# Optimization experiments

Hardware: AMD Instinct MI355X
Metric: run time of the kernel (lower is better)

The kernel has to match this reference:

```python
import jax, jax.numpy as jnp
import numpy as np

B, S, HIDDEN, HEADS = 2, 1024, 1024, 8
HEAD = HIDDEN // HEADS
EPS = 1e-5


def setup_inputs() -> dict:
    key = jax.random.key(0)
    ks = jax.random.split(key, 11)
    d = HEAD
    return {
        "X": jax.random.normal(ks[0], (B, S, HIDDEN), jnp.float32),
        "Wq": jax.random.normal(ks[1], (HEADS, d, d), jnp.float32) / d,
        "Wk": jax.random.normal(ks[2], (HEADS, d, d), jnp.float32) / d,
        "Wv": jax.random.normal(ks[3], (HEADS, d, d), jnp.float32) / d,
        "theta": jax.random.normal(ks[4], (HEADS, d), jnp.float32) / d,
        "gn_weight": jnp.ones((HIDDEN,), jnp.float32),
        "gn_bias": jnp.zeros((HIDDEN,), jnp.float32),
        "Wg_re": jax.random.normal(ks[5], (HIDDEN, HIDDEN), jnp.float32) / HIDDEN,
        "Wg_im": jax.random.normal(ks[6], (HIDDEN, HIDDEN), jnp.float32) / HIDDEN,
        "Wo_re": jax.random.normal(ks[7], (HIDDEN, HIDDEN), jnp.float32) / HIDDEN,
        "Wo_im": jax.random.normal(ks[8], (HIDDEN, HIDDEN), jnp.float32) / HIDDEN,
    }


def _head(Xh, Wq, Wk, Wv, theta, gamma):
    # Xh: [B, S, d] complex64; one retention head with decay gamma.
    c = Xh.dtype
    s = Xh.shape[1]
    ns = jnp.arange(1, s + 1, dtype=jnp.float32)
    phase = ns[:, None] * theta[None, :]            # [S, d]
    Theta = jnp.exp(1j * phase).astype(c)           # exp(i*n*theta)
    Q = (Xh @ Wq.astype(c)) * Theta[None]
    K = (Xh @ Wk.astype(c)) * jnp.conj(Theta)[None]
    V = Xh @ Wv.astype(c)
    diff = ns[:, None] - ns[None, :]                # n - m
    D = jnp.where(diff >= 0, gamma ** jnp.maximum(diff, 0.0), 0.0).astype(c)
    att = jnp.einsum('bnd,bmd->bnm', Q, K) * D[None]  # no conjugation (plain matmul, as in torch)
    return jnp.einsum('bnm,bmd->bnd', att, V)


def _group_norm(Y, w, b):
    # complex group norm: per-group complex mean, real variance E|x-mu|^2 (unbiased)
    Z = Y.reshape(-1, HEADS, HEAD)
    mu = Z.mean(axis=2, keepdims=True)
    dz = Z - mu
    var = (dz.real ** 2 + dz.imag ** 2).sum(axis=2, keepdims=True) / (HEAD - 1)
    Z = dz / jnp.sqrt(var + EPS).astype(Z.dtype)
    Z = Z.reshape(-1, HIDDEN)
    return Z * w + b


def _forward(X, Wq, Wk, Wv, theta, gn_weight, gn_bias, Wg_re, Wg_im, Wo_re, Wo_im):
    c = jnp.complex64
    Xc = X.astype(c)
    gammas = (1.0 - jnp.exp(jnp.linspace(np.log(1.0 / 32.0), np.log(1.0 / 512.0), HEADS))).astype(jnp.float32)
    Xh = Xc.reshape(B, S, HEADS, HEAD).transpose(2, 0, 1, 3)  # [H, B, S, d]
    Y = jax.vmap(_head)(Xh, Wq, Wk, Wv, theta, gammas)        # [H, B, S, d]
    Y = Y.transpose(1, 2, 0, 3).reshape(B, S, HIDDEN)         # concat heads
    Y = _group_norm(Y.reshape(-1, HIDDEN), gn_weight, gn_bias).reshape(B, S, HIDDEN)
    Wg = (Wg_re + 1j * Wg_im).astype(c)
    Wo = (Wo_re + 1j * Wo_im).astype(c)
    G = Xc @ Wg
    G = G * (1.0 / (1.0 + jnp.exp(-G)))                       # complex swish
    return (G + Y) @ Wo


def reference(X, Wq, Wk, Wv, theta, gn_weight, gn_bias, Wg_re, Wg_im, Wo_re, Wo_im):
    return _forward(X, Wq, Wk, Wv, theta, gn_weight, gn_bias, Wg_re, Wg_im, Wo_re, Wo_im)
```

## Files before the change

kernel.cpp:

```cpp
#include <hip/hip_runtime.h>
#include <math.h>

#define BATCH  2
#define SEQ    1024
#define HIDDEN 1024
#define NHEADS 8
#define DHEAD  128
#define NTOK   (BATCH*SEQ)
#define GEPS   1e-5f

typedef float f32x16 __attribute__((ext_vector_type(16)));
typedef __bf16 bf16x8 __attribute__((ext_vector_type(8)));
typedef unsigned int u32x4 __attribute__((ext_vector_type(4)));
typedef unsigned int u32x2 __attribute__((ext_vector_type(2)));

union Frag { u32x4 u; bf16x8 h; };

__device__ __forceinline__ unsigned short f2bf(float f) {
    unsigned int u = __float_as_uint(f);
    unsigned int r = (u + 0x7FFFu + ((u >> 16) & 1u)) >> 16;
    return (unsigned short)r;
}
__device__ __forceinline__ float bf2f(unsigned short u) {
    return __uint_as_float(((unsigned int)u) << 16);
}

__device__ __forceinline__ void cswish(float zr, float zi, float& outr, float& outi) {
    const float e = expf(-zr);
    float sg, cg;
    sincosf(zi, &sg, &cg);
    const float wr = fmaf(e, cg, 1.0f);
    const float wi = -e*sg;
    const float inv = 1.0f / fmaf(wr, wr, wi*wi);
    outr = (zr*wr + zi*wi)*inv;
    outi = (zi*wr - zr*wi)*inv;
}

__global__ __launch_bounds__(256) void prep_kernel(
    const float* __restrict__ X,
    const float* __restrict__ Wq, const float* __restrict__ Wk, const float* __restrict__ Wv,
    const float* __restrict__ Wgre, const float* __restrict__ Wgim,
    const float* __restrict__ Wore, const float* __restrict__ Woim,
    float* __restrict__ gpow, unsigned short* __restrict__ Xb,
    unsigned short* __restrict__ Wt, unsigned short* __restrict__ Bg,
    unsigned short* __restrict__ Bot)
{
    __shared__ float Ws[64][65];
    const int id  = blockIdx.x;
    const int tid = threadIdx.x;

    if (id < 32) {
        const int h = id >> 2;
        const int k = (id & 3)*256 + tid;
        const float l = fmaf((float)h, -0.39608410317711170f, -3.46573590279972650f);
        const float gamma = 1.0f - expf(l);
        gpow[h*SEQ + k] = powf(gamma, (float)k);
    } else if (id < 1056) {
        const size_t i = ((size_t)(id - 32)*256 + tid)*8;
        const float4 a = *(const float4*)&X[i];
        const float4 b = *(const float4*)&X[i+4];
        __align__(16) unsigned short t[8] = { f2bf(a.x), f2bf(a.y), f2bf(a.z), f2bf(a.w),
                                              f2bf(b.x), f2bf(b.y), f2bf(b.z), f2bf(b.w) };
        *(u32x4*)&Xb[i] = *(u32x4*)t;
    } else if (id < 1152) {
        const int q = id - 1056;
        const int th_ = q % 24, yy = q / 24;
        const int type = th_ >> 3, h = th_ & 7;
        const int k0 = (yy >> 1)*64, n0 = (yy & 1)*64;
        const float* W = ((type == 0) ? Wq : (type == 1) ? Wk : Wv)
                         + (size_t)h*DHEAD*DHEAD;
        #pragma unroll
        for (int it = 0; it < 4; ++it) {
            const int r = (tid >> 4) + it*16, c = (tid & 15)*4;
            *(float4*)&Ws[r][c] = *(const float4*)&W[(size_t)(k0 + r)*DHEAD + n0 + c];
        }
        __syncthreads();
        const int nl = tid >> 2, seg = (tid & 3)*16;
        __align__(16) unsigned short t[16];
        #pragma unroll
        for (int j = 0; j < 16; ++j) t[j] = f2bf(Ws[seg + j][nl]);
        u32x4* d = (u32x4*)&Wt[((size_t)th_*DHEAD + n0 + nl)*DHEAD + k0 + seg];
        d[0] = ((u32x4*)t)[0];
        d[1] = ((u32x4*)t)[1];
    } else if (id < 1664) {
        const int q = id - 1152;
        const int xx = q & 31, k0 = (q >> 5)*64;
        const int plane = xx >> 4;
        const int c0 = (xx & 15)*64;
        const float* src = plane ? Wgim : Wgre;
        #pragma unroll
        for (int it = 0; it < 4; ++it) {
            const int r = (tid >> 4) + it*16, c = (tid & 15)*4;
            *(float4*)&Ws[r][c] = *(const float4*)&src[(size_t)(k0 + r)*HIDDEN + c0 + c];
        }
        __syncthreads();
        const int nl = tid >> 2, seg = (tid & 3)*16;
        __align__(16) unsigned short t[16];
        #pragma unroll
        for (int j = 0; j < 16; ++j) t[j] = f2bf(Ws[seg + j][nl]);
        u32x4* d = (u32x4*)&Bg[((size_t)plane << 20) + (size_t)(c0 + nl)*HIDDEN + k0 + seg];
        d[0] = ((u32x4*)t)[0];
        d[1] = ((u32x4*)t)[1];
    } else {
        const int q = id - 1664;
        const int n0 = (q & 15)*64, k0 = (q >> 4)*64;
        const float* src;
        float sign = 1.0f;
        if (k0 < HIDDEN) src = Wore; else { src = Woim; sign = -1.0f; }
        const int kc = k0 & (HIDDEN-1);
        #pragma unroll
        for (int it = 0; it < 4; ++it) {
            const int r = (tid >> 4) + it*16, c = (tid & 15)*4;
            const float4 v = *(const float4*)&src[(size_t)(kc + r)*HIDDEN + n0 + c];
            Ws[r][c+0] = v.x*sign; Ws[r][c+1] = v.y*sign; Ws[r][c+2] = v.z*sign; Ws[r][c+3] = v.w*sign;
        }
        __syncthreads();
        const int nl = tid >> 2, seg = (tid & 3)*16;
        __align__(16) unsigned short t[16];
        #pragma unroll
        for (int j = 0; j < 16; ++j) t[j] = f2bf(Ws[seg + j][nl]);
        u32x4* d = (u32x4*)&Bot[(size_t)(n0 + nl)*(2*HIDDEN) + k0 + seg];
        d[0] = ((u32x4*)t)[0];
        d[1] = ((u32x4*)t)[1];
    }
}

__global__ __launch_bounds__(256) void projm_kernel(
    const unsigned short* __restrict__ Xb,
    const unsigned short* __restrict__ Wt,
    const float* __restrict__ theta,
    unsigned short* __restrict__ Qbre, unsigned short* __restrict__ Qbim,
    unsigned short* __restrict__ Kbre, unsigned short* __restrict__ Kbim,
    unsigned short* __restrict__ Vtb)
{
    const int tt = blockIdx.x;
    const int h  = blockIdx.y;
    const int mt = blockIdx.z;
    const int tid = threadIdx.x;
    const int w = tid >> 6, lane = tid & 63;
    const int th = w >> 1, nh = w & 1;
    const int l31 = lane & 31, hi = (lane >> 5) & 1;

    Frag A[8];
    {
        const unsigned short* xa = Xb + (size_t)(tt*64 + th*32 + l31)*HIDDEN
                                   + h*DHEAD + 8*hi;
        #pragma unroll
        for (int ks = 0; ks < 8; ++ks) A[ks].u = *(const u32x4*)(xa + 16*ks);
    }

    const unsigned short* wb = Wt + (size_t)(mt*NHEADS + h)*DHEAD*DHEAD;

    #pragma unroll
    for (int nt = 0; nt < 2; ++nt) {
        const int n0 = nh*64 + nt*32;
        const int n  = n0 + l31;

        Frag B[8];
        const unsigned short* wp = wb + (size_t)n*DHEAD + 8*hi;
        #pragma unroll
        for (int ks = 0; ks < 8; ++ks) B[ks].u = *(const u32x4*)(wp + 16*ks);

        f32x16 acc;
        #pragma unroll
        for (int e = 0; e < 16; ++e) acc[e] = 0.f;
        #pragma unroll
        for (int ks = 0; ks < 8; ++ks)
            acc = __builtin_amdgcn_mfma_f32_32x32x16_bf16(A[ks].h, B[ks].h, acc, 0, 0, 0);

        if (mt == 2) {
            const int b2  = (tt*64) >> 10;
            const int bh2 = b2*NHEADS + h;
            const int sbase = (tt*64 + th*32) & (SEQ-1);
            unsigned short* vdst = Vtb + ((size_t)(bh2*DHEAD + n))*SEQ + sbase;
            #pragma unroll
            for (int g2 = 0; g2 < 4; ++g2) {
                const int s0 = 8*g2 + 4*hi;
                __align__(8) unsigned short t4[4];
                #pragma unroll
                for (int j = 0; j < 4; ++j) t4[j] = f2bf(acc[g2*4 + j]);
                *(u32x2*)(vdst + s0) = *(u32x2*)t4;
            }
        } else {
            const float thv = theta[h*DHEAD + n];
            unsigned short* pre = (mt == 0) ? Qbre : Kbre;
            unsigned short* pim = (mt == 0) ? Qbim : Kbim;
            const float sgn = (mt == 0) ? 1.0f : -1.0f;
            #pragma unroll
            for (int r = 0; r < 16; ++r) {
                const int row = (r & 3) + 8*(r >> 2) + 4*hi;
                const int tok = tt*64 + th*32 + row;
                const float np1 = (float)((tok & (SEQ-1)) + 1);
                float s, c;
                sincosf(np1*thv, &s, &c);
                const size_t g = (size_t)tok*HIDDEN + h*DHEAD + n;
                pre[g] = f2bf(acc[r]*c);
                pim[g] = f2bf(acc[r]*s*sgn);
            }
        }
    }
}

#define CVTPK(dst, a, b) asm("v_cvt_pk_bf16_f32 %0, %1, %2" : "=v"(dst) : "v"(a), "v"(b))
#define SWAP32(x, y)     asm("v_permlane32_swap_b32 %0, %1" : "+v"(x), "+v"(y))

union FatLds {
    struct { float Ytr[32][133]; float Yti[32][133]; } a;
    struct { unsigned short As[64][68]; unsigned short Br[64][68]; unsigned short Bi[64][68]; } g;
};

__global__ __launch_bounds__(128) void fat_kernel(
    const unsigned short* __restrict__ Qbre, const unsigned short* __restrict__ Qbim,
    const unsigned short* __restrict__ Kbre, const unsigned short* __restrict__ Kbim,
    const unsigned short* __restrict__ Vtb,  const float* __restrict__ gpow,
    const float* __restrict__ gnw, const float* __restrict__ gnb,
    unsigned short* __restrict__ Yn,
    const unsigned short* __restrict__ Xb, const unsigned short* __restrict__ Bg,
    unsigned short* __restrict__ Gs)
{
    __shared__ FatLds lds;

    const int bid  = blockIdx.x;
    const int tid  = threadIdx.x;
    const int lane = tid & 63;
    const int wv   = tid >> 6;
    const int l31 = lane & 31, hi = (lane >> 5) & 1;

    if (bid < 512) {
        const int id = bid;
        const int bh = ((id & 7) << 1) | ((id >> 3) & 1);
        const int qt = id >> 4;

        const int b = bh >> 3, h = bh & 7;
        const int q0 = qt * 32;
        const size_t bhoff = (size_t)b*SEQ*HIDDEN + h*DHEAD;
        const float* gp = gpow + h*SEQ;

        int   crw[16];
        float ginv[16];
        #pragma unroll
        for (int r = 0; r < 16; ++r) {
            const int cr = (r & 3) + 8*(r >> 2) + 4*hi;
            crw[r] = cr;
            ginv[r] = 1.0f / gp[cr];
        }

        Frag Qr[8], Qi[8];
        {
            const unsigned short* qr = Qbre + bhoff + (size_t)(q0 + l31)*HIDDEN + 8*hi;
            const unsigned short* qi = Qbim + bhoff + (size_t)(q0 + l31)*HIDDEN + 8*hi;
            #pragma unroll
            for (int ks = 0; ks < 8; ++ks) {
                Qr[ks].u = *(const u32x4*)(qr + 16*ks);
                Qi[ks].u = *(const u32x4*)(qi + 16*ks);
            }
        }

        f32x16 Yr[4], Yi[4];
        #pragma unroll
        for (int dt = 0; dt < 4; ++dt)
            #pragma unroll
            for (int e = 0; e < 16; ++e) { Yr[dt][e] = 0.f; Yi[dt][e] = 0.f; }

        const int nm   = qt + 1;
        const int half = (nm + 1) >> 1;
        const int mlo  = wv ? half : 0;
        const int mhi  = wv ? nm   : half;

        #pragma unroll 1
        for (int m = mlo; m < mhi; ++m) {
            const int kv0 = m*32;

            Frag Kr[8], Ki[8];
            {
                const unsigned short* kr = Kbre + bhoff + (size_t)(kv0 + l31)*HIDDEN + 8*hi;
                const unsigned short* ki = Kbim + bhoff + (size_t)(kv0 + l31)*HIDDEN + 8*hi;
                #pragma unroll
                for (int ks = 0; ks < 8; ++ks) {
                    Kr[ks].u = *(const u32x4*)(kr + 16*ks);
                    Ki[ks].u = *(const u32x4*)(ki + 16*ks);
                }
            }
            Frag Vf[4][2];
            #pragma unroll
            for (int dt = 0; dt < 4; ++dt)
                #pragma unroll
                for (int ks2 = 0; ks2 < 2; ++ks2)
                    Vf[dt][ks2].u = *(const u32x4*)(Vtb + ((size_t)(bh*DHEAD + dt*32 + l31))*SEQ
                                                    + kv0 + 16*ks2 + 8*hi);

            const int  base = 32*(qt - m) + l31;
            const float g1  = gp[base];

            f32x16 SR, SI;
            #pragma unroll
            for (int e = 0; e < 16; ++e) { SR[e] = 0.f; SI[e] = 0.f; }
            #pragma unroll
            for (int ks = 0; ks < 8; ++ks) {
                Frag Qin;
                #pragma unroll
                for (int e = 0; e < 4; ++e) Qin.u[e] = Qi[ks].u[e] ^ 0x80008000u;
                SR = __builtin_amdgcn_mfma_f32_32x32x16_bf16(Kr[ks].h, Qr[ks].h, SR, 0, 0, 0);
                SI = __builtin_amdgcn_mfma_f32_32x32x16_bf16(Kr[ks].h, Qi[ks].h, SI, 0, 0, 0);
                SR = __builtin_amdgcn_mfma_f32_32x32x16_bf16(Ki[ks].h, Qin.h, SR, 0, 0, 0);
                SI = __builtin_amdgcn_mfma_f32_32x32x16_bf16(Ki[ks].h, Qr[ks].h, SI, 0, 0, 0);
            }

            float pr[16], pi[16];
            #pragma unroll
            for (int r = 0; r < 16; ++r) {
                const float w = (base >= crw[r]) ? g1*ginv[r] : 0.0f;
                pr[r] = SR[r]*w;
                pi[r] = SI[r]*w;
            }

            Frag PR[2], PI[2];
            #pragma unroll
            for (int ks2 = 0; ks2 < 2; ++ks2) {
                const int o = ks2*8;
                unsigned int a0, b0, a1, b1;
                CVTPK(a0, pr[o+0], pr[o+1]);
                CVTPK(b0, pr[o+4], pr[o+5]);
                SWAP32(a0, b0);
                CVTPK(a1, pr[o+2], pr[o+3]);
                CVTPK(b1, pr[o+6], pr[o+7]);
                SWAP32(a1, b1);
                PR[ks2].u[0] = a0; PR[ks2].u[1] = a1; PR[ks2].u[2] = b0; PR[ks2].u[3] = b1;
                CVTPK(a0, pi[o+0], pi[o+1]);
                CVTPK(b0, pi[o+4], pi[o+5]);
                SWAP32(a0, b0);
                CVTPK(a1, pi[o+2], pi[o+3]);
                CVTPK(b1, pi[o+6], pi[o+7]);
                SWAP32(a1, b1);
                PI[ks2].u[0] = a0; PI[ks2].u[1] = a1; PI[ks2].u[2] = b0; PI[ks2].u[3] = b1;
            }

            #pragma unroll
            for (int dt = 0; dt < 4; ++dt) {
                Yr[dt] = __builtin_amdgcn_mfma_f32_32x32x16_bf16(Vf[dt][0].h, PR[0].h, Yr[dt], 0, 0, 0);
                Yr[dt] = __builtin_amdgcn_mfma_f32_32x32x16_bf16(Vf[dt][1].h, PR[1].h, Yr[dt], 0, 0, 0);
                Yi[dt] = __builtin_amdgcn_mfma_f32_32x32x16_bf16(Vf[dt][0].h, PI[0].h, Yi[dt], 0, 0, 0);
                Yi[dt] = __builtin_amdgcn_mfma_f32_32x32x16_bf16(Vf[dt][1].h, PI[1].h, Yi[dt], 0, 0, 0);
            }
        }

        if (wv == 0) {
            #pragma unroll
            for (int dt = 0; dt < 4; ++dt)
                #pragma unroll
                for (int r = 0; r < 16; ++r) {
                    lds.a.Ytr[l31][dt*32 + crw[r]] = Yr[dt][r];
                    lds.a.Yti[l31][dt*32 + crw[r]] = Yi[dt][r];
                }
        }
        __syncthreads();
        if (wv == 1) {
            #pragma unroll
            for (int dt = 0; dt < 4; ++dt)
                #pragma unroll
                for (int r = 0; r < 16; ++r) {
                    lds.a.Ytr[l31][dt*32 + crw[r]] += Yr[dt][r];
                    lds.a.Yti[l31][dt*32 + crw[r]] += Yi[dt][r];
                }
        }
        __syncthreads();

        {
            const int row = tid >> 2;
            const int q4  = tid & 3;
            float sr = 0.f, si = 0.f;
            #pragma unroll 8
            for (int i = 0; i < 32; ++i) {
                sr += lds.a.Ytr[row][q4*32 + i];
                si += lds.a.Yti[row][q4*32 + i];
            }
            sr += __shfl_xor(sr, 1); sr += __shfl_xor(sr, 2);
            si += __shfl_xor(si, 1); si += __shfl_xor(si, 2);
            const float mr = sr * (1.0f/128.0f), mi = si * (1.0f/128.0f);
            float vs = 0.f;
            #pragma unroll 8
            for (int i = 0; i < 32; ++i) {
                const float dr = lds.a.Ytr[row][q4*32 + i] - mr;
                const float di = lds.a.Yti[row][q4*32 + i] - mi;
                vs = fmaf(dr, dr, vs);
                vs = fmaf(di, di, vs);
            }
            vs += __shfl_xor(vs, 1); vs += __shfl_xor(vs, 2);
            const float scale = 1.0f / sqrtf(vs * (1.0f/127.0f) + GEPS);

            unsigned short* dst = Yn + (size_t)(b*SEQ + q0 + row)*(2*HIDDEN) + h*DHEAD + q4*32;
            #pragma unroll
            for (int i = 0; i < 32; i += 8) {
                __align__(16) unsigned short tre[8], tim[8];
                #pragma unroll
                for (int e = 0; e < 8; ++e) {
                    const int col = q4*32 + i + e;
                    const float wv_ = gnw[h*DHEAD + col];
                    const float bv_ = gnb[h*DHEAD + col];
                    tre[e] = f2bf(fmaf((lds.a.Ytr[row][col] - mr)*scale, wv_, bv_));
                    tim[e] = f2bf((lds.a.Yti[row][col] - mi)*scale*wv_);
                }
                *(u32x4*)(dst + i)          = *(u32x4*)tre;
                *(u32x4*)(dst + HIDDEN + i) = *(u32x4*)tim;
            }
        }
    } else {
        const int gid = bid - 512;
        const int mb = gid >> 4;
        const int cb = gid & 15;
        const int wm = wv*32;

        const int arow = tid >> 1, aseg = (tid & 1)*32;
        const unsigned short* ga  = Xb + (size_t)(mb*64 + arow)*HIDDEN + aseg;
        const unsigned short* gbr = Bg + (size_t)(cb*64 + arow)*HIDDEN + aseg;
        const unsigned short* gbi = gbr + (1u << 20);

        f32x16 aR0, aR1, aI0, aI1;
        #pragma unroll
        for (int e = 0; e < 16; ++e) { aR0[e]=0.f; aR1[e]=0.f; aI0[e]=0.f; aI1[e]=0.f; }

        u32x4 ra0 = *(const u32x4*)(ga);
        u32x4 ra1 = *(const u32x4*)(ga + 8);
        u32x4 ra2 = *(const u32x4*)(ga + 16);
        u32x4 ra3 = *(const u32x4*)(ga + 24);
        u32x4 rr0 = *(const u32x4*)(gbr);
        u32x4 rr1 = *(const u32x4*)(gbr + 8);
        u32x4 rr2 = *(const u32x4*)(gbr + 16);
        u32x4 rr3 = *(const u32x4*)(gbr + 24);
        u32x4 ri0 = *(const u32x4*)(gbi);
        u32x4 ri1 = *(const u32x4*)(gbi + 8);
        u32x4 ri2 = *(const u32x4*)(gbi + 16);
        u32x4 ri3 = *(const u32x4*)(gbi + 24);

        for (int kk = 0; kk < HIDDEN; kk += 64) {
            __syncthreads();
            *(u32x4*)&lds.g.As[arow][aseg]      = ra0;
            *(u32x4*)&lds.g.As[arow][aseg + 8]  = ra1;
            *(u32x4*)&lds.g.As[arow][aseg + 16] = ra2;
            *(u32x4*)&lds.g.As[arow][aseg + 24] = ra3;
            *(u32x4*)&lds.g.Br[arow][aseg]      = rr0;
            *(u32x4*)&lds.g.Br[arow][aseg + 8]  = rr1;
            *(u32x4*)&lds.g.Br[arow][aseg + 16] = rr2;
            *(u32x4*)&lds.g.Br[arow][aseg + 24] = rr3;
            *(u32x4*)&lds.g.Bi[arow][aseg]      = ri0;
            *(u32x4*)&lds.g.Bi[arow][aseg + 8]  = ri1;
            *(u32x4*)&lds.g.Bi[arow][aseg + 16] = ri2;
            *(u32x4*)&lds.g.Bi[arow][aseg + 24] = ri3;
            if (kk + 64 < HIDDEN) {
                const int o = kk + 64;
                ra0 = *(const u32x4*)(ga + o);
                ra1 = *(const u32x4*)(ga + o + 8);
                ra2 = *(const u32x4*)(ga + o + 16);
                ra3 = *(const u32x4*)(ga + o + 24);
                rr0 = *(const u32x4*)(gbr + o);
                rr1 = *(const u32x4*)(gbr + o + 8);
                rr2 = *(const u32x4*)(gbr + o + 16);
                rr3 = *(const u32x4*)(gbr + o + 24);
                ri0 = *(const u32x4*)(gbi + o);
                ri1 = *(const u32x4*)(gbi + o + 8);
                ri2 = *(const u32x4*)(gbi + o + 16);
                ri3 = *(const u32x4*)(gbi + o + 24);
            }
            __syncthreads();
            #pragma unroll
            for (int ks = 0; ks < 4; ++ks) {
                Frag a, br0, br1, bi0, bi1;
                a.u   = *(const u32x4*)&lds.g.As[wm + l31][ks*16 + hi*8];
                br0.u = *(const u32x4*)&lds.g.Br[l31     ][ks*16 + hi*8];
                br1.u = *(const u32x4*)&lds.g.Br[l31 + 32][ks*16 + hi*8];
                bi0.u = *(const u32x4*)&lds.g.Bi[l31     ][ks*16 + hi*8];
                bi1.u = *(const u32x4*)&lds.g.Bi[l31 + 32][ks*16 + hi*8];
                aR0 = __builtin_amdgcn_mfma_f32_32x32x16_bf16(a.h, br0.h, aR0, 0, 0, 0);
                aR1 = __builtin_amdgcn_mfma_f32_32x32x16_bf16(a.h, br1.h, aR1, 0, 0, 0);
                aI0 = __builtin_amdgcn_mfma_f32_32x32x16_bf16(a.h, bi0.h, aI0, 0, 0, 0);
                aI1 = __builtin_amdgcn_mfma_f32_32x32x16_bf16(a.h, bi1.h, aI1, 0, 0, 0);
            }
        }

        #pragma unroll
        for (int ct = 0; ct < 2; ++ct) {
            const f32x16& cr = ct ? aR1 : aR0;
            const f32x16& ci = ct ? aI1 : aI0;
            const int c = cb*64 + ct*32 + l31;
            #pragma unroll
            for (int r = 0; r < 16; ++r) {
                const int row = mb*64 + wm + (r & 3) + 8*(r >> 2) + 4*hi;
                float swr, swi;
                cswish(cr[r], ci[r], swr, swi);
                const size_t o = (size_t)row*(2*HIDDEN) + c;
                Gs[o]          = f2bf(swr);
                Gs[o + HIDDEN] = f2bf(swi);
            }
        }
    }
}

__global__ __launch_bounds__(256) void zadd_kernel(
    const unsigned short* __restrict__ Gs, const unsigned short* __restrict__ Yn,
    unsigned short* __restrict__ Aout)
{
    const size_t i = ((size_t)blockIdx.x*256 + threadIdx.x)*8;
    const u32x4 g = *(const u32x4*)&Gs[i];
    const u32x4 y = *(const u32x4*)&Yn[i];
    __align__(16) unsigned short gg[8], yy[8], t[8];
    *(u32x4*)gg = g; *(u32x4*)yy = y;
    #pragma unroll
    for (int e = 0; e < 8; ++e) t[e] = f2bf(bf2f(gg[e]) + bf2f(yy[e]));
    *(u32x4*)&Aout[i] = *(u32x4*)t;
}

__global__ __launch_bounds__(256) void wprep_o_kernel(
    const float* __restrict__ Wore, const float* __restrict__ Woim,
    unsigned short* __restrict__ Bot, const int imMode)
{
    const int n0 = blockIdx.x*64, k0 = blockIdx.y*64;
    const float* src;
    float sign = 1.0f;
    if (!imMode) { if (k0 < HIDDEN) src = Wore; else { src = Woim; sign = -1.0f; } }
    else         { src = (k0 < HIDDEN) ? Woim : Wore; }
    const int kc = k0 & (HIDDEN-1);
    __shared__ float Ws[64][65];
    const int tid = threadIdx.x;
    #pragma unroll
    for (int it = 0; it < 4; ++it) {
        const int r = (tid >> 4) + it*16, c = (tid & 15)*4;
        const float4 v = *(const float4*)&src[(size_t)(kc + r)*HIDDEN + n0 + c];
        Ws[r][c+0] = v.x*sign; Ws[r][c+1] = v.y*sign; Ws[r][c+2] = v.z*sign; Ws[r][c+3] = v.w*sign;
    }
    __syncthreads();
    const int nl = tid >> 2, seg = (tid & 3)*16;
    __align__(16) unsigned short t[16];
    #pragma unroll
    for (int j = 0; j < 16; ++j) t[j] = f2bf(Ws[seg + j][nl]);
    u32x4* d = (u32x4*)&Bot[(size_t)(n0 + nl)*(2*HIDDEN) + k0 + seg];
    d[0] = ((u32x4*)t)[0];
    d[1] = ((u32x4*)t)[1];
}

__global__ __launch_bounds__(256) void ogemm_kernel(
    const unsigned short* __restrict__ A,
    const unsigned short* __restrict__ Bt,
    float* __restrict__ C, const int mode)
{
    const int K = 2*HIDDEN, N = HIDDEN;
    __shared__ __align__(16) unsigned short As[128][72];
    __shared__ __align__(16) unsigned short Bs[64][72];

    const int tid = threadIdx.x;
    const int mb = blockIdx.x, nb = blockIdx.y;
    const int lane = tid & 63, w = tid >> 6;
    const int l31 = lane & 31, hi = (lane >> 5) & 1;
    const int wm = w*32;

    const int arow = tid >> 1, aseg = (tid & 1)*32;
    const int brow = tid >> 2, bseg = (tid & 3)*16;

    const unsigned short* ga = A  + (size_t)(mb*128 + arow)*K + aseg;
    const unsigned short* gb = Bt + (size_t)(nb*64 + brow)*K + bseg;

    f32x16 acc0, acc1;
    #pragma unroll
    for (int e = 0; e < 16; ++e) { acc0[e]=0.f; acc1[e]=0.f; }

    u32x4 ra0 = *(const u32x4*)(ga);
    u32x4 ra1 = *(const u32x4*)(ga + 8);
    u32x4 ra2 = *(const u32x4*)(ga + 16);
    u32x4 ra3 = *(const u32x4*)(ga + 24);
    u32x4 rb0 = *(const u32x4*)(gb);
    u32x4 rb1 = *(const u32x4*)(gb + 8);

    for (int kk = 0; kk < K; kk += 64) {
        __syncthreads();
        *(u32x4*)&As[arow][aseg]      = ra0;
        *(u32x4*)&As[arow][aseg + 8]  = ra1;
        *(u32x4*)&As[arow][aseg + 16] = ra2;
        *(u32x4*)&As[arow][aseg + 24] = ra3;
        *(u32x4*)&Bs[brow][bseg]      = rb0;
        *(u32x4*)&Bs[brow][bseg + 8]  = rb1;
        if (kk + 64 < K) {
            const int o = kk + 64;
            ra0 = *(const u32x4*)(ga + o);
            ra1 = *(const u32x4*)(ga + o + 8);
            ra2 = *(const u32x4*)(ga + o + 16);
            ra3 = *(const u32x4*)(ga + o + 24);
            rb0 = *(const u32x4*)(gb + o);
            rb1 = *(const u32x4*)(gb + o + 8);
        }
        __syncthreads();
        #pragma unroll
        for (int ks = 0; ks < 4; ++ks) {
            Frag a, b0, b1;
            a.u  = *(const u32x4*)&As[wm + l31][ks*16 + hi*8];
            b0.u = *(const u32x4*)&Bs[l31     ][ks*16 + hi*8];
            b1.u = *(const u32x4*)&Bs[l31 + 32][ks*16 + hi*8];
            acc0 = __builtin_amdgcn_mfma_f32_32x32x16_bf16(a.h, b0.h, acc0, 0, 0, 0);
            acc1 = __builtin_amdgcn_mfma_f32_32x32x16_bf16(a.h, b1.h, acc1, 0, 0, 0);
        }
    }

    const int cb = nb*64 + l31;
    #pragma unroll
    for (int r = 0; r < 16; ++r) {
        const int row = mb*128 + wm + (r & 3) + 8*(r >> 2) + 4*hi;
        if (mode == 0) {
            float* cr = C + (size_t)row*N + cb;
            cr[0]  = acc0[r];
            cr[32] = acc1[r];
        } else {
            float* cr = C + ((size_t)row*N + cb)*2 + (mode - 1);
            cr[0]  = acc0[r];
            cr[64] = acc1[r];
        }
    }
}

extern "C" void kernel_launch(void* const* d_in, const int* in_sizes, int n_in,
                              void* d_out, int out_size, void* d_ws, size_t ws_size,
                              hipStream_t stream)
{
    (void)in_sizes; (void)n_in; (void)ws_size;

    const float* X     = (const float*)d_in[0];
    const float* Wq    = (const float*)d_in[1];
    const float* Wk    = (const float*)d_in[2];
    const float* Wv    = (const float*)d_in[3];
    const float* theta = (const float*)d_in[4];
    const float* gnw   = (const float*)d_in[5];
    const float* gnb   = (const float*)d_in[6];
    const float* Wgre  = (const float*)d_in[7];
    const float* Wgim  = (const float*)d_in[8];
    const float* Wore  = (const float*)d_in[9];
    const float* Woim  = (const float*)d_in[10];

    float* ws = (float*)d_ws;
    const size_t P = (size_t)NTOK*HIDDEN;

    unsigned short* Yn   = (unsigned short*)ws;
    unsigned short* Bot  = (unsigned short*)(ws + P);
    unsigned short* Qbre = (unsigned short*)(ws + 2*P);
    unsigned short* Qbim = Qbre + P;
    unsigned short* Kbre = Qbim + P;
    unsigned short* Kbim = Kbre + P;
    unsigned short* Aout = Qbre;
    unsigned short* Gs   = (unsigned short*)(ws + 4*P);
    unsigned short* Vtb  = (unsigned short*)(ws + 5*P);
    unsigned short* Xb   = (unsigned short*)(ws + 5*P) + P;
    unsigned short* Bg   = (unsigned short*)(ws + 6*P);
    unsigned short* Wt   = (unsigned short*)(ws + 6*P) + P;
    unsigned short* Boti = Wt;
    float* gpw = ws + 7*P;

    const int cplx = (out_size >= (int)(2*P)) ? 1 : 0;

    hipLaunchKernelGGL(prep_kernel, dim3(2176), dim3(256), 0, stream,
                       X, Wq, Wk, Wv, Wgre, Wgim, Wore, Woim,
                       gpw, Xb, Wt, Bg, Bot);
    hipLaunchKernelGGL(projm_kernel, dim3(NTOK/64, NHEADS, 3), dim3(256), 0, stream,
                       Xb, Wt, theta, Qbre, Qbim, Kbre, Kbim, Vtb);

    hipLaunchKernelGGL(fat_kernel, dim3(1024), dim3(128), 0, stream,
                       Qbre, Qbim, Kbre, Kbim, Vtb, gpw, gnw, gnb, Yn, Xb, Bg, Gs);

    hipLaunchKernelGGL(zadd_kernel, dim3(2048), dim3(256), 0, stream, Gs, Yn, Aout);

    if (!cplx) {
        hipLaunchKernelGGL(ogemm_kernel, dim3(NTOK/128, HIDDEN/64), dim3(256), 0, stream,
                           Aout, Bot, (float*)d_out, 0);
    } else {
        hipLaunchKernelGGL(wprep_o_kernel, dim3(HIDDEN/64, 2*HIDDEN/64), dim3(256), 0, stream,
                           Wore, Woim, Boti, 1);
        hipLaunchKernelGGL(ogemm_kernel, dim3(NTOK/128, HIDDEN/64), dim3(256), 0, stream,
                           Aout, Bot, (float*)d_out, 1);
        hipLaunchKernelGGL(ogemm_kernel, dim3(NTOK/128, HIDDEN/64), dim3(256), 0, stream,
                           Aout, Boti, (float*)d_out, 2);
    }
}
```

Before: 122.4 us.

## Restructure fat kernel to 4-wave blocks with paired causal tiles and K prefetch

The retention part now uses 256-thread blocks. Each block handles a complementary pair of query tiles (j and 31-j) to balance causal work, and splits the KV range across four waves. K fragments for the next KV tile are loaded early so the loads overlap the MFMAs. The gate GEMM part is re-split into 2x2 waves per 64x64 tile with a swizzled column-block order, and the grid drops from 1024 to 768 blocks. In exchange, the four-wave LDS reduction adds more syncthreads, and larger blocks may lower occupancy.

```diff
diff --git a/kernel.cpp b/kernel.cpp
--- a/kernel.cpp
+++ b/kernel.cpp
@@ -209,7 +209,7 @@
     struct { unsigned short As[64][68]; unsigned short Br[64][68]; unsigned short Bi[64][68]; } g;
 };
 
-__global__ __launch_bounds__(128) void fat_kernel(
+__global__ __launch_bounds__(256) void fat_kernel(
     const unsigned short* __restrict__ Qbre, const unsigned short* __restrict__ Qbim,
     const unsigned short* __restrict__ Kbre, const unsigned short* __restrict__ Kbim,
     const unsigned short* __restrict__ Vtb,  const float* __restrict__ gpow,
@@ -226,13 +226,10 @@
     const int wv   = tid >> 6;
     const int l31 = lane & 31, hi = (lane >> 5) & 1;
 
-    if (bid < 512) {
-        const int id = bid;
-        const int bh = ((id & 7) << 1) | ((id >> 3) & 1);
-        const int qt = id >> 4;
-
+    if (bid < 256) {
+        const int bh = ((bid & 7) << 1) | ((bid >> 3) & 1);
+        const int j  = bid >> 4;
         const int b = bh >> 3, h = bh & 7;
-        const int q0 = qt * 32;
         const size_t bhoff = (size_t)b*SEQ*HIDDEN + h*DHEAD;
         const float* gp = gpow + h*SEQ;
 
@@ -245,248 +242,264 @@
             ginv[r] = 1.0f / gp[cr];
         }
 
-        Frag Qr[8], Qi[8];
-        {
-            const unsigned short* qr = Qbre + bhoff + (size_t)(q0 + l31)*HIDDEN + 8*hi;
-            const unsigned short* qi = Qbim + bhoff + (size_t)(q0 + l31)*HIDDEN + 8*hi;
-            #pragma unroll
-            for (int ks = 0; ks < 8; ++ks) {
-                Qr[ks].u = *(const u32x4*)(qr + 16*ks);
-                Qi[ks].u = *(const u32x4*)(qi + 16*ks);
-            }
-        }
-
-        f32x16 Yr[4], Yi[4];
-        #pragma unroll
-        for (int dt = 0; dt < 4; ++dt)
-            #pragma unroll
-            for (int e = 0; e < 16; ++e) { Yr[dt][e] = 0.f; Yi[dt][e] = 0.f; }
-
-        const int nm   = qt + 1;
-        const int half = (nm + 1) >> 1;
-        const int mlo  = wv ? half : 0;
-        const int mhi  = wv ? nm   : half;
-
         #pragma unroll 1
-        for (int m = mlo; m < mhi; ++m) {
-            const int kv0 = m*32;
-
-            Frag Kr[8], Ki[8];
+        for (int tile = 0; tile < 2; ++tile) {
+            const int qt = tile ? (31 - j) : j;
+            const int q0 = qt * 32;
+
+            Frag Qr[8], Qi[8];
             {
-                const unsigned short* kr = Kbre + bhoff + (size_t)(kv0 + l31)*HIDDEN + 8*hi;
-                const unsigned short* ki = Kbim + bhoff + (size_t)(kv0 + l31)*HIDDEN + 8*hi;
+                const unsigned short* qr = Qbre + bhoff + (size_t)(q0 + l31)*HIDDEN + 8*hi;
+                const unsigned short* qi = Qbim + bhoff + (size_t)(q0 + l31)*HIDDEN + 8*hi;
                 #pragma unroll
                 for (int ks = 0; ks < 8; ++ks) {
-                    Kr[ks].u = *(const u32x4*)(kr + 16*ks);
-                    Ki[ks].u = *(const u32x4*)(ki + 16*ks);
-                }
-            }
-            Frag Vf[4][2];
+                    Qr[ks].u = *(const u32x4*)(qr + 16*ks);
+                    Qi[ks].u = *(const u32x4*)(qi + 16*ks);
+                }
+            }
+
+            f32x16 Yr[4], Yi[4];
             #pragma unroll
             for (int dt = 0; dt < 4; ++dt)
                 #pragma unroll
-                for (int ks2 = 0; ks2 < 2; ++ks2)
-                    Vf[dt][ks2].u = *(const u32x4*)(Vtb + ((size_t)(bh*DHEAD + dt*32 + l31))*SEQ
-                                                    + kv0 + 16*ks2 + 8*hi);
-
-            const int  base = 32*(qt - m) + l31;
-            const float g1  = gp[base];
-
-            f32x16 SR, SI;
-            #pragma unroll
-            for (int e = 0; e < 16; ++e) { SR[e] = 0.f; SI[e] = 0.f; }
-            #pragma unroll
-            for (int ks = 0; ks < 8; ++ks) {
-                Frag Qin;
-                #pragma unroll
-                for (int e = 0; e < 4; ++e) Qin.u[e] = Qi[ks].u[e] ^ 0x80008000u;
-                SR = __builtin_amdgcn_mfma_f32_32x32x16_bf16(Kr[ks].h, Qr[ks].h, SR, 0, 0, 0);
-                SI = __builtin_amdgcn_mfma_f32_32x32x16_bf16(Kr[ks].h, Qi[ks].h, SI, 0, 0, 0);
-                SR = __builtin_amdgcn_mfma_f32_32x32x16_bf16(Ki[ks].h, Qin.h, SR, 0, 0, 0);
-                SI = __builtin_amdgcn_mfma_f32_32x32x16_bf16(Ki[ks].h, Qr[ks].h, SI, 0, 0, 0);
-            }
-
-            float pr[16], pi[16];
-            #pragma unroll
-            for (int r = 0; r < 16; ++r) {
-                const float w = (base >= crw[r]) ? g1*ginv[r] : 0.0f;
-                pr[r] = SR[r]*w;
-                pi[r] = SI[r]*w;
-            }
-
-            Frag PR[2], PI[2];
-            #pragma unroll
-            for (int ks2 = 0; ks2 < 2; ++ks2) {
-                const int o = ks2*8;
-                unsigned int a0, b0, a1, b1;
-                CVTPK(a0, pr[o+0], pr[o+1]);
-                CVTPK(b0, pr[o+4], pr[o+5]);
-                SWAP32(a0, b0);
-                CVTPK(a1, pr[o+2], pr[o+3]);
-                CVTPK(b1, pr[o+6], pr[o+7]);
-                SWAP32(a1, b1);
-                PR[ks2].u[0] = a0; PR[ks2].u[1] = a1; PR[ks2].u[2] = b0; PR[ks2].u[3] = b1;
-                CVTPK(a0, pi[o+0], pi[o+1]);
-                CVTPK(b0, pi[o+4], pi[o+5]);
-                SWAP32(a0, b0);
-                CVTPK(a1, pi[o+2], pi[o+3]);
-                CVTPK(b1, pi[o+6], pi[o+7]);
-                SWAP32(a1, b1);
-                PI[ks2].u[0] = a0; PI[ks2].u[1] = a1; PI[ks2].u[2] = b0; PI[ks2].u[3] = b1;
-            }
-
-            #pragma unroll
-            for (int dt = 0; dt < 4; ++dt) {
-                Yr[dt] = __builtin_amdgcn_mfma_f32_32x32x16_bf16(Vf[dt][0].h, PR[0].h, Yr[dt], 0, 0, 0);
-                Yr[dt] = __builtin_amdgcn_mfma_f32_32x32x16_bf16(Vf[dt][1].h, PR[1].h, Yr[dt], 0, 0, 0);
-                Yi[dt] = __builtin_amdgcn_mfma_f32_32x32x16_bf16(Vf[dt][0].h, PI[0].h, Yi[dt], 0, 0, 0);
-                Yi[dt] = __builtin_amdgcn_mfma_f32_32x32x16_bf16(Vf[dt][1].h, PI[1].h, Yi[dt], 0, 0, 0);
-            }
-        }
-
-        if (wv == 0) {
-            #pragma unroll
-            for (int dt = 0; dt < 4; ++dt)
+                for (int e = 0; e < 16; ++e) { Yr[dt][e] = 0.f; Yi[dt][e] = 0.f; }
+
+            const int nm  = qt + 1;
+            const int mlo = (nm * wv) >> 2;
+            const int mhi = (nm * (wv + 1)) >> 2;
+
+            Frag Kr[8], Ki[8];
+            if (mlo < mhi) {
+                const int kv0p = mlo*32;
+                const unsigned short* kr_ = Kbre + bhoff + (size_t)(kv0p + l31)*HIDDEN + 8*hi;
+                const unsigned short* ki_ = Kbim + bhoff + (size_t)(kv0p + l31)*HIDDEN + 8*hi;
+                #pragma unroll
+                for (int ks = 0; ks < 8; ++ks) {
+                    Kr[ks].u = *(const u32x4*)(kr_ + 16*ks);
+                    Ki[ks].u = *(const u32x4*)(ki_ + 16*ks);
+                }
+            }
+
+            #pragma unroll 1
+            for (int m = mlo; m < mhi; ++m) {
+                const int kv0 = m*32;
+
+                Frag Vf[4][2];
+                #pragma unroll
+                for (int dt = 0; dt < 4; ++dt)
+                    #pragma unroll
+                    for (int ks2 = 0; ks2 < 2; ++ks2)
+                        Vf[dt][ks2].u = *(const u32x4*)(Vtb + ((size_t)(bh*DHEAD + dt*32 + l31))*SEQ
+                                                        + kv0 + 16*ks2 + 8*hi);
+
+                const int  base = 32*(qt - m) + l31;
+                const float g1  = gp[base];
+
+                f32x16 SR, SI;
+                #pragma unroll
+                for (int e = 0; e < 16; ++e) { SR[e] = 0.f; SI[e] = 0.f; }
+                #pragma unroll
+                for (int ks = 0; ks < 8; ++ks) {
+                    Frag Qin;
+                    #pragma unroll
+                    for (int e = 0; e < 4; ++e) Qin.u[e] = Qi[ks].u[e] ^ 0x80008000u;
+                    SR = __builtin_amdgcn_mfma_f32_32x32x16_bf16(Kr[ks].h, Qr[ks].h, SR, 0, 0, 0);
+                    SI = __builtin_amdgcn_mfma_f32_32x32x16_bf16(Kr[ks].h, Qi[ks].h, SI, 0, 0, 0);
+                    SR = __builtin_amdgcn_mfma_f32_32x32x16_bf16(Ki[ks].h, Qin.h, SR, 0, 0, 0);
+                    SI = __builtin_amdgcn_mfma_f32_32x32x16_bf16(Ki[ks].h, Qr[ks].h, SI, 0, 0, 0);
+                }
+
+                if (m + 1 < mhi) {
+                    const int kn = (m + 1)*32;
+                    const unsigned short* kr_ = Kbre + bhoff + (size_t)(kn + l31)*HIDDEN + 8*hi;
+                    const unsigned short* ki_ = Kbim + bhoff + (size_t)(kn + l31)*HIDDEN + 8*hi;
+                    #pragma unroll
+                    for (int ks = 0; ks < 8; ++ks) {
+                        Kr[ks].u = *(const u32x4*)(kr_ + 16*ks);
+                        Ki[ks].u = *(const u32x4*)(ki_ + 16*ks);
+                    }
+                }
+
+                float pr[16], pi[16];
                 #pragma unroll
                 for (int r = 0; r < 16; ++r) {
-                    lds.a.Ytr[l31][dt*32 + crw[r]] = Yr[dt][r];
-                    lds.a.Yti[l31][dt*32 + crw[r]] = Yi[dt][r];
-                }
-        }
-        __syncthreads();
-        if (wv == 1) {
-            #pragma unroll
-            for (int dt = 0; dt < 4; ++dt)
-                #pragma unroll
-                for (int r = 0; r < 16; ++r) {
-                    lds.a.Ytr[l31][dt*32 + crw[r]] += Yr[dt][r];
-                    lds.a.Yti[l31][dt*32 + crw[r]] += Yi[dt][r];
-                }
-        }
-        __syncthreads();
-
-        {
-            const int row = tid >> 2;
-            const int q4  = tid & 3;
-            float sr = 0.f, si = 0.f;
-            #pragma unroll 8
-            for (int i = 0; i < 32; ++i) {
-                sr += lds.a.Ytr[row][q4*32 + i];
-                si += lds.a.Yti[row][q4*32 + i];
-            }
-            sr += __shfl_xor(sr, 1); sr += __shfl_xor(sr, 2);
-            si += __shfl_xor(si, 1); si += __shfl_xor(si, 2);
-            const float mr = sr * (1.0f/128.0f), mi = si * (1.0f/128.0f);
-            float vs = 0.f;
-            #pragma unroll 8
-            for (int i = 0; i < 32; ++i) {
-                const float dr = lds.a.Ytr[row][q4*32 + i] - mr;
-                const float di = lds.a.Yti[row][q4*32 + i] - mi;
-                vs = fmaf(dr, dr, vs);
-                vs = fmaf(di, di, vs);
-            }
-            vs += __shfl_xor(vs, 1); vs += __shfl_xor(vs, 2);
-            const float scale = 1.0f / sqrtf(vs * (1.0f/127.0f) + GEPS);
-
-            unsigned short* dst = Yn + (size_t)(b*SEQ + q0 + row)*(2*HIDDEN) + h*DHEAD + q4*32;
-            #pragma unroll
-            for (int i = 0; i < 32; i += 8) {
-                __align__(16) unsigned short tre[8], tim[8];
-                #pragma unroll
-                for (int e = 0; e < 8; ++e) {
-                    const int col = q4*32 + i + e;
-                    const float wv_ = gnw[h*DHEAD + col];
-                    const float bv_ = gnb[h*DHEAD + col];
-                    tre[e] = f2bf(fmaf((lds.a.Ytr[row][col] - mr)*scale, wv_, bv_));
-                    tim[e] = f2bf((lds.a.Yti[row][col] - mi)*scale*wv_);
-                }
-                *(u32x4*)(dst + i)          = *(u32x4*)tre;
-                *(u32x4*)(dst + HIDDEN + i) = *(u32x4*)tim;
+                    const float w = (base >= crw[r]) ? g1*ginv[r] : 0.0f;
+                    pr[r] = SR[r]*w;
+                    pi[r] = SI[r]*w;
+                }
+
+                Frag PR[2], PI[2];
+                #pragma unroll
+                for (int ks2 = 0; ks2 < 2; ++ks2) {
+                    const int o = ks2*8;
+                    unsigned int a0, b0, a1, b1;
+                    CVTPK(a0, pr[o+0], pr[o+1]);
+                    CVTPK(b0, pr[o+4], pr[o+5]);
+                    SWAP32(a0, b0);
+                    CVTPK(a1, pr[o+2], pr[o+3]);
+                    CVTPK(b1, pr[o+6], pr[o+7]);
+                    SWAP32(a1, b1);
+                    PR[ks2].u[0] = a0; PR[ks2].u[1] = a1; PR[ks2].u[2] = b0; PR[ks2].u[3] = b1;
+                    CVTPK(a0, pi[o+0], pi[o+1]);
+                    CVTPK(b0, pi[o+4], pi[o+5]);
+                    SWAP32(a0, b0);
+                    CVTPK(a1, pi[o+2], pi[o+3]);
+                    CVTPK(b1, pi[o+6], pi[o+7]);
+                    SWAP32(a1, b1);
+                    PI[ks2].u[0] = a0; PI[ks2].u[1] = a1; PI[ks2].u[2] = b0; PI[ks2].u[3] = b1;
+                }
+
+                #pragma unroll
+                for (int dt = 0; dt < 4; ++dt) {
+                    Yr[dt] = __builtin_amdgcn_mfma_f32_32x32x16_bf16(Vf[dt][0].h, PR[0].h, Yr[dt], 0, 0, 0);
+                    Yr[dt] = __builtin_amdgcn_mfma_f32_32x32x16_bf16(Vf[dt][1].h, PR[1].h, Yr[dt], 0, 0, 0);
+                    Yi[dt] = __builtin_amdgcn_mfma_f32_32x32x16_bf16(Vf[dt][0].h, PI[0].h, Yi[dt], 0, 0, 0);
+                    Yi[dt] = __builtin_amdgcn_mfma_f32_32x32x16_bf16(Vf[dt][1].h, PI[1].h, Yi[dt], 0, 0, 0);
+                }
+            }
+
+            __syncthreads();
+            if (wv == 0) {
+                #pragma unroll
+                for (int dt = 0; dt < 4; ++dt)
+                    #pragma unroll
+                    for (int r = 0; r < 16; ++r) {
+                        lds.a.Ytr[l31][dt*32 + crw[r]] = Yr[dt][r];
+                        lds.a.Yti[l31][dt*32 + crw[r]] = Yi[dt][r];
+                    }
+            }
+            __syncthreads();
+            if (wv == 1) {
+                #pragma unroll
+                for (int dt = 0; dt < 4; ++dt)
+                    #pragma unroll
+                    for (int r = 0; r < 16; ++r) {
+                        lds.a.Ytr[l31][dt*32 + crw[r]] += Yr[dt][r];
+                        lds.a.Yti[l31][dt*32 + crw[r]] += Yi[dt][r];
+                    }
+            }
+            __syncthreads();
+            if (wv == 2) {
+                #pragma unroll
+                for (int dt = 0; dt < 4; ++dt)
+                    #pragma unroll
+                    for (int r = 0; r < 16; ++r) {
+                        lds.a.Ytr[l31][dt*32 + crw[r]] += Yr[dt][r];
+                        lds.a.Yti[l31][dt*32 + crw[r]] += Yi[dt][r];
+                    }
+            }
+            __syncthreads();
+            if (wv == 3) {
+                #pragma unroll
+                for (int dt = 0; dt < 4; ++dt)
+                    #pragma unroll
+                    for (int r = 0; r < 16; ++r) {
+                        lds.a.Ytr[l31][dt*32 + crw[r]] += Yr[dt][r];
+                        lds.a.Yti[l31][dt*32 + crw[r]] += Yi[dt][r];
+                    }
+            }
+            __syncthreads();
+
+            {
+                const int row = tid >> 3;
+                const int q8  = tid & 7;
+                float sr = 0.f, si = 0.f;
+                #pragma unroll 8
+                for (int i = 0; i < 16; ++i) {
+                    sr += lds.a.Ytr[row][q8*16 + i];
+                    si += lds.a.Yti[row][q8*16 + i];
+                }
+                sr += __shfl_xor(sr, 1); sr += __shfl_xor(sr, 2); sr += __shfl_xor(sr, 4);
+                si += __shfl_xor(si, 1); si += __shfl_xor(si, 2); si += __shfl_xor(si, 4);
+                const float mr = sr * (1.0f/128.0f), mi = si * (1.0f/128.0f);
+                float vs = 0.f;
+                #pragma unroll 8
+                for (int i = 0; i < 16; ++i) {
+                    const float dr = lds.a.Ytr[row][q8*16 + i] - mr;
+                    const float di = lds.a.Yti[row][q8*16 + i] - mi;
+                    vs = fmaf(dr, dr, vs);
+                    vs = fmaf(di, di, vs);
+                }
+                vs += __shfl_xor(vs, 1); vs += __shfl_xor(vs, 2); vs += __shfl_xor(vs, 4);
+                const float scale = 1.0f / sqrtf(vs * (1.0f/127.0f) + GEPS);
+
+                unsigned short* dst = Yn + (size_t)(b*SEQ + q0 + row)*(2*HIDDEN) + h*DHEAD + q8*16;
+                #pragma unroll
+                for (int i = 0; i < 16; i += 8) {
+                    __align__(16) unsigned short tre[8], tim[8];
+                    #pragma unroll
+                    for (int e = 0; e < 8; ++e) {
+                        const int col = q8*16 + i + e;
+                        const float wv_ = gnw[h*DHEAD + col];
+                        const float bv_ = gnb[h*DHEAD + col];
+                        tre[e] = f2bf(fmaf((lds.a.Ytr[row][col] - mr)*scale, wv_, bv_));
+                        tim[e] = f2bf((lds.a.Yti[row][col] - mi)*scale*wv_);
+                    }
+                    *(u32x4*)(dst + i)          = *(u32x4*)tre;
+                    *(u32x4*)(dst + HIDDEN + i) = *(u32x4*)tim;
+                }
             }
         }
     } else {
-        const int gid = bid - 512;
+        const int gid = bid - 256;
+        const int cb = ((gid & 7) << 1) | ((gid >> 3) & 1);
         const int mb = gid >> 4;
-        const int cb = gid & 15;
-        const int wm = wv*32;
-
-        const int arow = tid >> 1, aseg = (tid & 1)*32;
-        const unsigned short* ga  = Xb + (size_t)(mb*64 + arow)*HIDDEN + aseg;
-        const unsigned short* gbr = Bg + (size_t)(cb*64 + arow)*HIDDEN + aseg;
+        const int wm  = (wv >> 1)*32;
+        const int wn_ = (wv & 1)*32;
+
+        const int r0  = tid >> 2;
+        const int seg = (tid & 3)*16;
+        const unsigned short* ga  = Xb + (size_t)(mb*64 + r0)*HIDDEN + seg;
+        const unsigned short* gbr = Bg + (size_t)(cb*64 + r0)*HIDDEN + seg;
         const unsigned short* gbi = gbr + (1u << 20);
 
-        f32x16 aR0, aR1, aI0, aI1;
-        #pragma unroll
-        for (int e = 0; e < 16; ++e) { aR0[e]=0.f; aR1[e]=0.f; aI0[e]=0.f; aI1[e]=0.f; }
+        f32x16 aR, aI;
+        #pragma unroll
+        for (int e = 0; e < 16; ++e) { aR[e]=0.f; aI[e]=0.f; }
 
         u32x4 ra0 = *(const u32x4*)(ga);
         u32x4 ra1 = *(const u32x4*)(ga + 8);
-        u32x4 ra2 = *(const u32x4*)(ga + 16);
-        u32x4 ra3 = *(const u32x4*)(ga + 24);
         u32x4 rr0 = *(const u32x4*)(gbr);
         u32x4 rr1 = *(const u32x4*)(gbr + 8);
-        u32x4 rr2 = *(const u32x4*)(gbr + 16);
-        u32x4 rr3 = *(const u32x4*)(gbr + 24);
         u32x4 ri0 = *(const u32x4*)(gbi);
         u32x4 ri1 = *(const u32x4*)(gbi + 8);
-        u32x4 ri2 = *(const u32x4*)(gbi + 16);
-        u32x4 ri3 = *(const u32x4*)(gbi + 24);
 
         for (int kk = 0; kk < HIDDEN; kk += 64) {
             __syncthreads();
-            *(u32x4*)&lds.g.As[arow][aseg]      = ra0;
-            *(u32x4*)&lds.g.As[arow][aseg + 8]  = ra1;
-            *(u32x4*)&lds.g.As[arow][aseg + 16] = ra2;
-            *(u32x4*)&lds.g.As[arow][aseg + 24] = ra3;
-            *(u32x4*)&lds.g.Br[arow][aseg]      = rr0;
-            *(u32x4*)&lds.g.Br[arow][aseg + 8]  = rr1;
-            *(u32x4*)&lds.g.Br[arow][aseg + 16] = rr2;
-            *(u32x4*)&lds.g.Br[arow][aseg + 24] = rr3;
-            *(u32x4*)&lds.g.Bi[arow][aseg]      = ri0;
-            *(u32x4*)&lds.g.Bi[arow][aseg + 8]  = ri1;
-            *(u32x4*)&lds.g.Bi[arow][aseg + 16] = ri2;
-            *(u32x4*)&lds.g.Bi[arow][aseg + 24] = ri3;
+            *(u32x4*)&lds.g.As[r0][seg]     = ra0;
+            *(u32x4*)&lds.g.As[r0][seg + 8] = ra1;
+            *(u32x4*)&lds.g.Br[r0][seg]     = rr0;
+            *(u32x4*)&lds.g.Br[r0][seg + 8] = rr1;
+            *(u32x4*)&lds.g.Bi[r0][seg]     = ri0;
+            *(u32x4*)&lds.g.Bi[r0][seg + 8] = ri1;
             if (kk + 64 < HIDDEN) {
                 const int o = kk + 64;
                 ra0 = *(const u32x4*)(ga + o);
                 ra1 = *(const u32x4*)(ga + o + 8);
-                ra2 = *(const u32x4*)(ga + o + 16);
-                ra3 = *(const u32x4*)(ga + o + 24);
                 rr0 = *(const u32x4*)(gbr + o);
                 rr1 = *(const u32x4*)(gbr + o + 8);
-                rr2 = *(const u32x4*)(gbr + o + 16);
-                rr3 = *(const u32x4*)(gbr + o + 24);
                 ri0 = *(const u32x4*)(gbi + o);
                 ri1 = *(const u32x4*)(gbi + o + 8);
-                ri2 = *(const u32x4*)(gbi + o + 16);
-                ri3 = *(const u32x4*)(gbi + o + 24);
             }
             __syncthreads();
             #pragma unroll
             for (int ks = 0; ks < 4; ++ks) {
-                Frag a, br0, br1, bi0, bi1;
-                a.u   = *(const u32x4*)&lds.g.As[wm + l31][ks*16 + hi*8];
-                br0.u = *(const u32x4*)&lds.g.Br[l31     ][ks*16 + hi*8];
-                br1.u = *(const u32x4*)&lds.g.Br[l31 + 32][ks*16 + hi*8];
-                bi0.u = *(const u32x4*)&lds.g.Bi[l31     ][ks*16 + hi*8];
-                bi1.u = *(const u32x4*)&lds.g.Bi[l31 + 32][ks*16 + hi*8];
-                aR0 = __builtin_amdgcn_mfma_f32_32x32x16_bf16(a.h, br0.h, aR0, 0, 0, 0);
-                aR1 = __builtin_amdgcn_mfma_f32_32x32x16_bf16(a.h, br1.h, aR1, 0, 0, 0);
-                aI0 = __builtin_amdgcn_mfma_f32_32x32x16_bf16(a.h, bi0.h, aI0, 0, 0, 0);
-                aI1 = __builtin_amdgcn_mfma_f32_32x32x16_bf16(a.h, bi1.h, aI1, 0, 0, 0);
-            }
-        }
-
-        #pragma unroll
-        for (int ct = 0; ct < 2; ++ct) {
-            const f32x16& cr = ct ? aR1 : aR0;
-            const f32x16& ci = ct ? aI1 : aI0;
-            const int c = cb*64 + ct*32 + l31;
+                Frag a, br, bi;
+                a.u  = *(const u32x4*)&lds.g.As[wm + l31 ][ks*16 + hi*8];
+                br.u = *(const u32x4*)&lds.g.Br[wn_ + l31][ks*16 + hi*8];
+                bi.u = *(const u32x4*)&lds.g.Bi[wn_ + l31][ks*16 + hi*8];
+                aR = __builtin_amdgcn_mfma_f32_32x32x16_bf16(a.h, br.h, aR, 0, 0, 0);
+                aI = __builtin_amdgcn_mfma_f32_32x32x16_bf16(a.h, bi.h, aI, 0, 0, 0);
+            }
+        }
+
+        {
+            const int c = cb*64 + wn_ + l31;
             #pragma unroll
             for (int r = 0; r < 16; ++r) {
                 const int row = mb*64 + wm + (r & 3) + 8*(r >> 2) + 4*hi;
                 float swr, swi;
-                cswish(cr[r], ci[r], swr, swi);
+                cswish(aR[r], aI[r], swr, swi);
                 const size_t o = (size_t)row*(2*HIDDEN) + c;
                 Gs[o]          = f2bf(swr);
                 Gs[o + HIDDEN] = f2bf(swi);
@@ -658,7 +671,7 @@
     hipLaunchKernelGGL(projm_kernel, dim3(NTOK/64, NHEADS, 3), dim3(256), 0, stream,
                        Xb, Wt, theta, Qbre, Qbim, Kbre, Kbim, Vtb);
 
-    hipLaunchKernelGGL(fat_kernel, dim3(1024), dim3(128), 0, stream,
+    hipLaunchKernelGGL(fat_kernel, dim3(768), dim3(256), 0, stream,
                        Qbre, Qbim, Kbre, Kbim, Vtb, gpw, gnw, gnb, Yn, Xb, Bg, Gs);
 
     hipLaunchKernelGGL(zadd_kernel, dim3(2048), dim3(256), 0, stream, Gs, Yn, Aout);
```

New measurement: 132.1 us. 1.08x slower.
